# Kernel tuning notes

Measured on AMD Instinct MI355X. Metric: run time of the kernel, lower is better.

## Reference

```python
import jax, jax.numpy as jnp
import numpy as np


def setup_inputs() -> dict:
    key = jax.random.key(0)
    k1, k2, k3, k4 = jax.random.split(key, 4)
    B, T, E, H = 16, 2048, 1024, 128
    x = jax.random.normal(k1, (B, T, E), dtype=jnp.float32)
    Wk = jax.random.normal(k2, (E, H), dtype=jnp.float32) * (E ** -0.5)
    Wq = jax.random.normal(k3, (E, H), dtype=jnp.float32) * (E ** -0.5)
    Wv = jax.random.normal(k4, (E, H), dtype=jnp.float32) * (E ** -0.5)
    return {"x": x, "Wk": Wk, "Wq": Wq, "Wv": Wv}


def reference(x, Wk, Wq, Wv):
    # x: [B,T,E]; Wk/Wq/Wv: [E,H]
    B, T, E = x.shape
    H = Wk.shape[1]
    k = jnp.einsum('bte,eh->bth', x, Wk)
    q = jnp.einsum('bte,eh->bth', x, Wq)
    v = jnp.einsum('bte,eh->bth', x, Wv)
    # scores [B,T,T]; original masks with -inf THEN scales (equivalent math)
    scores = jnp.einsum('bqh,bkh->bqk', q, k) * (H ** -0.5)
    causal = jnp.tril(jnp.ones((T, T), dtype=bool))
    scores = jnp.where(causal, scores, -jnp.inf)
    weights = jax.nn.softmax(scores, axis=-1)
    # dropout disabled (eval mode reference)
    return jnp.einsum('bqk,bkh->bqh', weights, v)
```

## Files before the change

### kernel.cpp

```cpp
#include <hip/hip_runtime.h>

#define B_ 16
#define T_ 2048
#define E_ 1024
#define H_ 128

typedef short bf16x8 __attribute__((ext_vector_type(8)));
typedef float f32x4 __attribute__((ext_vector_type(4)));
typedef unsigned short u16x4 __attribute__((ext_vector_type(4)));

static __device__ __forceinline__ unsigned short f2bf(float f) {
    unsigned int u = __float_as_uint(f);
    u += 0x7FFFu + ((u >> 16) & 1u);
    return (unsigned short)(u >> 16);
}
static __device__ __forceinline__ unsigned int pk2(unsigned short a, unsigned short b) {
    return (unsigned int)a | ((unsigned int)b << 16);
}
static __device__ __forceinline__ bf16x8 frag(uint4 v) {
    return __builtin_bit_cast(bf16x8, v);
}
static __device__ __forceinline__ void gl16(const unsigned short* g, unsigned short* l) {
    __builtin_amdgcn_global_load_lds(
        (const __attribute__((address_space(1))) void*)g,
        (__attribute__((address_space(3))) void*)l, 16, 0, 0);
}

__global__ __launch_bounds__(256) void cvtw_kernel(
    const float* __restrict__ w0, const float* __restrict__ w1,
    const float* __restrict__ w2, unsigned short* __restrict__ wt)
{
    int g   = blockIdx.x * 256 + threadIdx.x;
    int arr = g >> 14;
    int rem = g & 16383;
    int h   = rem >> 7;
    int e0  = (rem & 127) * 8;
    const float* src = (arr == 0) ? w0 : (arr == 1) ? w1 : w2;
    unsigned short b[8];
#pragma unroll
    for (int i = 0; i < 8; i++) b[i] = f2bf(src[(size_t)(e0 + i) * H_ + h]);
    uint4 o;
    o.x = pk2(b[0], b[1]); o.y = pk2(b[2], b[3]);
    o.z = pk2(b[4], b[5]); o.w = pk2(b[6], b[7]);
    *(uint4*)&wt[(size_t)(arr * 128 + h) * E_ + e0] = o;
}

__global__ __launch_bounds__(512, 4) void proj_kernel(
    const float* __restrict__ x,
    const unsigned short* __restrict__ wt,
    unsigned short* __restrict__ q_ws,
    unsigned short* __restrict__ kp_ws,
    unsigned short* __restrict__ vt_ws)
{
    const int m0 = blockIdx.x * 64;
    __shared__ __align__(16) unsigned short As[2][64 * 32];

    const int tid  = threadIdx.x;
    const int lane = tid & 63;
    const int w    = tid >> 6;
    const int quad = lane >> 4;
    const int lm   = lane & 15;
    const int wc   = w * 48;

    const int srow = tid >> 3;
    const int scol = (tid & 7) * 4;
    const float* gx = x + (size_t)(m0 + srow) * E_ + scol;
    const unsigned short* gb = wt + (size_t)(wc + lm) * E_ + quad * 8;

    const f32x4 z4 = {0.f, 0.f, 0.f, 0.f};
    f32x4 acc[4][3];
#pragma unroll
    for (int i = 0; i < 4; i++)
#pragma unroll
        for (int j = 0; j < 3; j++) acc[i][j] = z4;

    auto writeA = [&](float4 v, int buf) {
        u16x4 o;
        o[0] = f2bf(v.x); o[1] = f2bf(v.y);
        o[2] = f2bf(v.z); o[3] = f2bf(v.w);
        *(u16x4*)&As[buf][srow * 32 + scol] = o;
    };

    float4 a = *(const float4*)gx;
    writeA(a, 0);
    a = *(const float4*)(gx + 32);

    for (int kb = 0; kb < 32; kb++) {
        const int cb = kb & 1;
        __syncthreads();

        uint4 b0 = *(const uint4*)(gb + (size_t)kb * 32);
        uint4 b1 = *(const uint4*)(gb + (size_t)16 * E_ + (size_t)kb * 32);
        uint4 b2 = *(const uint4*)(gb + (size_t)32 * E_ + (size_t)kb * 32);

        const int kb2 = (kb + 2 < 32) ? kb + 2 : 31;
        float4 n = *(const float4*)(gx + kb2 * 32);
        if (kb + 1 < 32) writeA(a, cb ^ 1);

        bf16x8 af[4];
#pragma unroll
        for (int am = 0; am < 4; am++)
            af[am] = frag(*(const uint4*)&As[cb][(am * 16 + lm) * 32 + quad * 8]);

        const bf16x8 bf0 = frag(b0), bf1 = frag(b1), bf2 = frag(b2);
#pragma unroll
        for (int am = 0; am < 4; am++) {
            acc[am][0] = __builtin_amdgcn_mfma_f32_16x16x32_bf16(af[am], bf0, acc[am][0], 0, 0, 0);
            acc[am][1] = __builtin_amdgcn_mfma_f32_16x16x32_bf16(af[am], bf1, acc[am][1], 0, 0, 0);
            acc[am][2] = __builtin_amdgcn_mfma_f32_16x16x32_bf16(af[am], bf2, acc[am][2], 0, 0, 0);
        }
        a = n;
    }

#pragma unroll
    for (int am = 0; am < 4; am++)
#pragma unroll
        for (int bn = 0; bn < 3; bn++) {
            const int gcol  = wc + bn * 16 + lm;
            const int sel   = gcol >> 7;
            const int c     = gcol & 127;
            const int rbase = m0 + am * 16 + quad * 4;
            const int bb    = rbase >> 11;
            const int t     = rbase & 2047;
            if (sel == 0) {
#pragma unroll
                for (int r = 0; r < 4; r++)
                    q_ws[(size_t)(rbase + r) * H_ + c] = f2bf(acc[am][bn][r]);
            } else if (sel == 1) {
#pragma unroll
                for (int r = 0; r < 4; r++) {
                    int tt = t + r;
                    kp_ws[(size_t)(bb * 64 + (tt >> 5)) * 4096 +
                          (c >> 5) * 1024 + (tt & 31) * 32 + (c & 31)] =
                        f2bf(acc[am][bn][r]);
                }
            } else {
                u16x4 pv;
#pragma unroll
                for (int r = 0; r < 4; r++) pv[r] = f2bf(acc[am][bn][r]);
                *(u16x4*)&vt_ws[((size_t)(bb * 64 + (t >> 5)) * 128 + c) * 32 + (t & 31)] = pv;
            }
        }
}

__global__ __launch_bounds__(256, 2) void attn_kernel(
    const unsigned short* __restrict__ q_ws,
    const unsigned short* __restrict__ kp_ws,
    const unsigned short* __restrict__ vt_ws,
    float* __restrict__ out)
{
    __shared__ __align__(16) unsigned short Ks[2][4096];
    __shared__ __align__(16) unsigned short Vs[2][4096];
    __shared__ __align__(16) unsigned short Ps[4][16][40];

    const int bid   = blockIdx.x;
    const int batch = bid & 15;
    const int p     = (bid >> 4) & 15;
    const int tau   = (bid >> 8) ? (31 - p) : p;
    const int nkt   = 2 * tau + 2;

    const int tid  = threadIdx.x;
    const int lane = tid & 63;
    const int ww   = tid >> 6;
    const int quad = lane >> 4;
    const int lm   = lane & 15;
    const float scale = 0.08838834764831845f;

    bf16x8 ones;
#pragma unroll
    for (int i = 0; i < 8; i++) ones[i] = (short)0x3F80;
    const f32x4 z4 = {0.f, 0.f, 0.f, 0.f};

    const size_t bq = (size_t)batch * T_ * H_;
    const int so = ww * 1024 + lane * 8;
    const unsigned short* Kt = kp_ws + (size_t)(batch * 64) * 4096 + so;
    const unsigned short* Vt = vt_ws + (size_t)(batch * 64) * 4096 + so;

    bf16x8 qf[4];
#pragma unroll
    for (int h = 0; h < 4; h++)
        qf[h] = frag(*(const uint4*)(q_ws + bq +
                 (size_t)(tau * 64 + ww * 16 + lm) * H_ + h * 32 + quad * 8));

    f32x4 o[9];
#pragma unroll
    for (int f = 0; f < 9; f++) o[f] = z4;

    gl16(Kt, &Ks[0][ww * 1024]); gl16(Kt + 512, &Ks[0][ww * 1024 + 512]);
    gl16(Vt, &Vs[0][ww * 1024]); gl16(Vt + 512, &Vs[0][ww * 1024 + 512]);

    for (int kt = 0; kt < nkt; kt++) {
        const int cb = kt & 1;
        __syncthreads();

        if (kt + 1 < nkt) {
            const int nb = cb ^ 1;
            const unsigned short* kg = Kt + (size_t)(kt + 1) * 4096;
            const unsigned short* vg = Vt + (size_t)(kt + 1) * 4096;
            gl16(kg, &Ks[nb][ww * 1024]); gl16(kg + 512, &Ks[nb][ww * 1024 + 512]);
            gl16(vg, &Vs[nb][ww * 1024]); gl16(vg + 512, &Vs[nb][ww * 1024 + 512]);
        }

        f32x4 st0 = z4, st1 = z4;
        __builtin_amdgcn_s_setprio(1);
#pragma unroll
        for (int h = 0; h < 4; h++) {
            bf16x8 kf0 = frag(*(const uint4*)&Ks[cb][(h * 32 + lm) * 32 + quad * 8]);
            bf16x8 kf1 = frag(*(const uint4*)&Ks[cb][(h * 32 + 16 + lm) * 32 + quad * 8]);
            st0 = __builtin_amdgcn_mfma_f32_16x16x32_bf16(kf0, qf[h], st0, 0, 0, 0);
            st1 = __builtin_amdgcn_mfma_f32_16x16x32_bf16(kf1, qf[h], st1, 0, 0, 0);
        }
        __builtin_amdgcn_s_setprio(0);

        const int qg = tau * 64 + ww * 16 + lm;
        const int k0 = kt * 32;
        u16x4 pa, pb;
#pragma unroll
        for (int r = 0; r < 4; r++) {
            int kv0 = k0 + quad * 4 + r;
            float e0 = __expf(st0[r] * scale);
            float e1 = __expf(st1[r] * scale);
            pa[r] = (kv0      <= qg) ? f2bf(e0) : (unsigned short)0;
            pb[r] = (kv0 + 16 <= qg) ? f2bf(e1) : (unsigned short)0;
        }
        *(u16x4*)&Ps[ww][lm][quad * 4]      = pa;
        *(u16x4*)&Ps[ww][lm][16 + quad * 4] = pb;
        bf16x8 pf = frag(*(const uint4*)&Ps[ww][lm][quad * 8]);

        __builtin_amdgcn_s_setprio(1);
#pragma unroll
        for (int f = 0; f < 8; f++) {
            bf16x8 vfr = frag(*(const uint4*)&Vs[cb][(f * 16 + lm) * 32 + quad * 8]);
            o[f] = __builtin_amdgcn_mfma_f32_16x16x32_bf16(pf, vfr, o[f], 0, 0, 0);
        }
        o[8] = __builtin_amdgcn_mfma_f32_16x16x32_bf16(pf, ones, o[8], 0, 0, 0);
        __builtin_amdgcn_s_setprio(0);
    }

    float* op = out + bq + (size_t)(tau * 64 + ww * 16) * H_;
#pragma unroll
    for (int r = 0; r < 4; r++) {
        float inv = 1.f / o[8][r];
#pragma unroll
        for (int f = 0; f < 8; f++)
            op[(size_t)(quad * 4 + r) * H_ + f * 16 + lm] = o[f][r] * inv;
    }
}

extern "C" void kernel_launch(void* const* d_in, const int* in_sizes, int n_in,
                              void* d_out, int out_size, void* d_ws, size_t ws_size,
                              hipStream_t stream)
{
    const float* x  = (const float*)d_in[0];
    const float* Wk = (const float*)d_in[1];
    const float* Wq = (const float*)d_in[2];
    const float* Wv = (const float*)d_in[3];
    float* out = (float*)d_out;

    const size_t MH = (size_t)B_ * T_ * H_;
    unsigned short* q_ws  = (unsigned short*)d_ws;
    unsigned short* kp_ws = q_ws + MH;
    unsigned short* vt_ws = kp_ws + MH;
    unsigned short* wt    = vt_ws + MH;

    cvtw_kernel<<<dim3(192), dim3(256), 0, stream>>>(Wq, Wk, Wv, wt);
    proj_kernel<<<dim3(512), dim3(512), 0, stream>>>(x, wt, q_ws, kp_ws, vt_ws);
    attn_kernel<<<dim3(512), dim3(256), 0, stream>>>(q_ws, kp_ws, vt_ws, out);
}
```

Measured before the change: 288.3 us.

## Stage projection weights via LDS and triple-buffer K/V tiles in attention

```diff
diff --git a/kernel.cpp b/kernel.cpp
--- a/kernel.cpp
+++ b/kernel.cpp
@@ -54,6 +54,7 @@
 {
     const int m0 = blockIdx.x * 64;
     __shared__ __align__(16) unsigned short As[2][64 * 32];
+    __shared__ __align__(16) unsigned short Bs[2][384 * 32];
 
     const int tid  = threadIdx.x;
     const int lane = tid & 63;
@@ -62,10 +63,13 @@
     const int lm   = lane & 15;
     const int wc   = w * 48;
 
-    const int srow = tid >> 3;
-    const int scol = (tid & 7) * 4;
-    const float* gx = x + (size_t)(m0 + srow) * E_ + scol;
-    const unsigned short* gb = wt + (size_t)(wc + lm) * E_ + quad * 8;
+    const int arow = tid >> 3;
+    const int acol = (tid & 7) * 4;
+    const float* gx = x + (size_t)(m0 + arow) * E_ + acol;
+
+    const int brow = tid >> 2;
+    const int bcol = (tid & 3) * 8;
+    const unsigned short* gw = wt + (size_t)brow * E_ + bcol;
 
     const f32x4 z4 = {0.f, 0.f, 0.f, 0.f};
     f32x4 acc[4][3];
@@ -74,14 +78,22 @@
 #pragma unroll
         for (int j = 0; j < 3; j++) acc[i][j] = z4;
 
+    auto stageB = [&](int kb, int buf) {
+        const unsigned short* g = gw + kb * 32;
+        unsigned short* l = &Bs[buf][tid * 8];
+        gl16(g,                    l);
+        gl16(g + (size_t)128 * E_, l + 4096);
+        gl16(g + (size_t)256 * E_, l + 8192);
+    };
     auto writeA = [&](float4 v, int buf) {
         u16x4 o;
         o[0] = f2bf(v.x); o[1] = f2bf(v.y);
         o[2] = f2bf(v.z); o[3] = f2bf(v.w);
-        *(u16x4*)&As[buf][srow * 32 + scol] = o;
+        *(u16x4*)&As[buf][arow * 32 + acol] = o;
     };
 
     float4 a = *(const float4*)gx;
+    stageB(0, 0);
     writeA(a, 0);
     a = *(const float4*)(gx + 32);
 
@@ -89,26 +101,27 @@
         const int cb = kb & 1;
         __syncthreads();
 
-        uint4 b0 = *(const uint4*)(gb + (size_t)kb * 32);
-        uint4 b1 = *(const uint4*)(gb + (size_t)16 * E_ + (size_t)kb * 32);
-        uint4 b2 = *(const uint4*)(gb + (size_t)32 * E_ + (size_t)kb * 32);
-
         const int kb2 = (kb + 2 < 32) ? kb + 2 : 31;
         float4 n = *(const float4*)(gx + kb2 * 32);
-        if (kb + 1 < 32) writeA(a, cb ^ 1);
-
-        bf16x8 af[4];
+        if (kb + 1 < 32) {
+            stageB(kb + 1, cb ^ 1);
+            writeA(a, cb ^ 1);
+        }
+
+        bf16x8 af[4], bf[3];
 #pragma unroll
         for (int am = 0; am < 4; am++)
             af[am] = frag(*(const uint4*)&As[cb][(am * 16 + lm) * 32 + quad * 8]);
-
-        const bf16x8 bf0 = frag(b0), bf1 = frag(b1), bf2 = frag(b2);
-#pragma unroll
-        for (int am = 0; am < 4; am++) {
-            acc[am][0] = __builtin_amdgcn_mfma_f32_16x16x32_bf16(af[am], bf0, acc[am][0], 0, 0, 0);
-            acc[am][1] = __builtin_amdgcn_mfma_f32_16x16x32_bf16(af[am], bf1, acc[am][1], 0, 0, 0);
-            acc[am][2] = __builtin_amdgcn_mfma_f32_16x16x32_bf16(af[am], bf2, acc[am][2], 0, 0, 0);
-        }
+#pragma unroll
+        for (int bn = 0; bn < 3; bn++)
+            bf[bn] = frag(*(const uint4*)&Bs[cb][(wc + bn * 16 + lm) * 32 + quad * 8]);
+#pragma unroll
+        for (int am = 0; am < 4; am++)
+#pragma unroll
+            for (int bn = 0; bn < 3; bn++)
+                acc[am][bn] = __builtin_amdgcn_mfma_f32_16x16x32_bf16(
+                    af[am], bf[bn], acc[am][bn], 0, 0, 0);
+
         a = n;
     }
 
@@ -149,8 +162,8 @@
     const unsigned short* __restrict__ vt_ws,
     float* __restrict__ out)
 {
-    __shared__ __align__(16) unsigned short Ks[2][4096];
-    __shared__ __align__(16) unsigned short Vs[2][4096];
+    __shared__ __align__(16) unsigned short Ks[3][4096];
+    __shared__ __align__(16) unsigned short Vs[3][4096];
     __shared__ __align__(16) unsigned short Ps[4][16][40];
 
     const int bid   = blockIdx.x;
@@ -176,6 +189,15 @@
     const unsigned short* Kt = kp_ws + (size_t)(batch * 64) * 4096 + so;
     const unsigned short* Vt = vt_ws + (size_t)(batch * 64) * 4096 + so;
 
+    auto stage = [&](int t, int b) {
+        const unsigned short* kg = Kt + (size_t)t * 4096;
+        const unsigned short* vg = Vt + (size_t)t * 4096;
+        gl16(kg,       &Ks[b][ww * 1024]);
+        gl16(kg + 512, &Ks[b][ww * 1024 + 512]);
+        gl16(vg,       &Vs[b][ww * 1024]);
+        gl16(vg + 512, &Vs[b][ww * 1024 + 512]);
+    };
+
     bf16x8 qf[4];
 #pragma unroll
     for (int h = 0; h < 4; h++)
@@ -186,20 +208,18 @@
 #pragma unroll
     for (int f = 0; f < 9; f++) o[f] = z4;
 
-    gl16(Kt, &Ks[0][ww * 1024]); gl16(Kt + 512, &Ks[0][ww * 1024 + 512]);
-    gl16(Vt, &Vs[0][ww * 1024]); gl16(Vt + 512, &Vs[0][ww * 1024 + 512]);
+    stage(0, 0);
+    stage(1, 1);
 
     for (int kt = 0; kt < nkt; kt++) {
-        const int cb = kt & 1;
-        __syncthreads();
-
-        if (kt + 1 < nkt) {
-            const int nb = cb ^ 1;
-            const unsigned short* kg = Kt + (size_t)(kt + 1) * 4096;
-            const unsigned short* vg = Vt + (size_t)(kt + 1) * 4096;
-            gl16(kg, &Ks[nb][ww * 1024]); gl16(kg + 512, &Ks[nb][ww * 1024 + 512]);
-            gl16(vg, &Vs[nb][ww * 1024]); gl16(vg + 512, &Vs[nb][ww * 1024 + 512]);
-        }
+        const int cb = kt % 3;
+        asm volatile("s_waitcnt vmcnt(4) lgkmcnt(0)" ::: "memory");
+        __builtin_amdgcn_sched_barrier(0);
+        __builtin_amdgcn_s_barrier();
+        __builtin_amdgcn_sched_barrier(0);
+
+        int ks = kt + 2; if (ks > nkt - 1) ks = nkt - 1;
+        stage(ks, (kt + 2) % 3);
 
         f32x4 st0 = z4, st1 = z4;
         __builtin_amdgcn_s_setprio(1);
```

Measured after the change: 283.7 us. No clear change (-1.6%).
